# Optimization experiments

Measured on AMD Instinct MI355X. Metric: run time of the kernel, lower is better.

Reference implementation:

```python
import jax, jax.numpy as jnp
import numpy as np

B, S, C, H = 2, 2048, 1024, 16
D = C // H  # head_size = 64


def setup_inputs() -> dict:
    key = jax.random.key(0)
    ks = jax.random.split(key, 8)
    scale = 1.0 / np.sqrt(C)
    return {
        "src": jax.random.normal(ks[0], (B, S, C), dtype=jnp.float32),
        "Wq": jax.random.normal(ks[1], (C, C), dtype=jnp.float32) * scale,
        "bq": jnp.zeros((C,), dtype=jnp.float32),
        "Wk": jax.random.normal(ks[2], (C, C), dtype=jnp.float32) * scale,
        "bk": jnp.zeros((C,), dtype=jnp.float32),
        "Wv": jax.random.normal(ks[3], (C, C), dtype=jnp.float32) * scale,
        "bv": jnp.zeros((C,), dtype=jnp.float32),
        "rel_k_table": jax.random.normal(ks[4], (2 * S - 1, D), dtype=jnp.float32),
    }


def reference(src, Wq, bq, Wk, bk, Wv, bv, rel_k_table):
    # Linear projections (torch Linear: x @ W.T + b)
    q = src @ Wq.T + bq  # (B,S,C)
    k = src @ Wk.T + bk
    v = src @ Wv.T + bv
    # Faithful to torch .view: raw reshape (B,S,C) -> (B,H,S,D), NOT a transpose split
    q = q.reshape(B, H, S, D)
    k = k.reshape(B, H, S, D)
    v = v.reshape(B, H, S, D)
    # content score: q @ k^T
    content = jnp.einsum("bhsd,bhtd->bhst", q, k)  # (B,H,S,S)
    # relative-position embeddings: (S,S,D)
    pos = jnp.arange(S)
    shifted = pos[None, :] - pos[:, None] + (S - 1)  # (S,S) in [0, 2S-2]
    rel_k = rel_k_table[shifted]  # (S,S,D)
    # q.view(S, B*H, D) @ rel_k.permute(0,2,1): batched over first (query-pos) axis
    q_r = q.reshape(S, B * H, D)
    pos_score = jnp.einsum("sbd,std->sbt", q_r, rel_k)  # (S,BH,S)
    pos_score = jnp.transpose(pos_score, (1, 0, 2)).reshape(B, H, S, S)
    scores = (content + pos_score) / jnp.sqrt(jnp.float32(D))
    attn = jax.nn.softmax(scores, axis=-1)
    out = jnp.einsum("bhst,bhtd->bhsd", attn, v)  # (B,H,S,D)
    out = jnp.transpose(out, (0, 2, 1, 3)).reshape(B, S, C)
    return out
```

## Files before the change

kernel.cpp:

```cpp
#include <hip/hip_runtime.h>
#include <hip/hip_bf16.h>

#define BATCH 2
#define SEQ   2048
#define CH    1024
#define NH    16
#define HD    64
#define BHN   (BATCH*NH)
#define SD    (SEQ*HD)

typedef short v8s __attribute__((ext_vector_type(8)));
typedef short v4s __attribute__((ext_vector_type(4)));
typedef float v4f __attribute__((ext_vector_type(4)));

#define VMCNT2() asm volatile("s_waitcnt vmcnt(2)" ::: "memory")
#define VMCNT0() asm volatile("s_waitcnt vmcnt(0)" ::: "memory")
#define SBAR()  do { __builtin_amdgcn_sched_barrier(0); \
                     __builtin_amdgcn_s_barrier();      \
                     __builtin_amdgcn_sched_barrier(0); } while (0)

__device__ __forceinline__ short f2bf(float f) {
    unsigned u = __float_as_uint(f);
    u += 0x7fff + ((u >> 16) & 1);
    return (short)(u >> 16);
}

__device__ __forceinline__ unsigned pk2bf(float a, float b) {
    __hip_bfloat162 h = __float22bfloat162_rn(make_float2(a, b));
    unsigned u;
    __builtin_memcpy(&u, &h, 4);
    return u;
}

__device__ __forceinline__ float ex2(float x) {
    float r; asm("v_exp_f32 %0, %1" : "=v"(r) : "v"(x)); return r;
}

__device__ __forceinline__ void gl_lds16(const short* g, short* l) {
    __builtin_amdgcn_global_load_lds(
        (const __attribute__((address_space(1))) void*)g,
        (__attribute__((address_space(3))) void*)l, 16, 0, 0);
}

__global__ __launch_bounds__(256) void cast_all_kernel(
    const float* __restrict__ src, const float* __restrict__ wq,
    const float* __restrict__ wk, const float* __restrict__ wv,
    const float* __restrict__ rel,
    short* __restrict__ xb, short* __restrict__ wqb,
    short* __restrict__ wkb, short* __restrict__ wvb,
    short* __restrict__ relb)
{
    const int z = blockIdx.z;
    const float* s; short* d; int n4;
    switch (z) {
        case 0: s = src; d = xb;   n4 = 1048576; break;
        case 1: s = wq;  d = wqb;  n4 = 262144;  break;
        case 2: s = wk;  d = wkb;  n4 = 262144;  break;
        case 3: s = wv;  d = wvb;  n4 = 262144;  break;
        default: s = rel; d = relb; n4 = 65520;  break;
    }
    for (int i = blockIdx.x * 256 + threadIdx.x; i < n4; i += gridDim.x * 256) {
        float4 v = ((const float4*)s)[i];
        v4s o; o.x = f2bf(v.x); o.y = f2bf(v.y); o.z = f2bf(v.z); o.w = f2bf(v.w);
        ((v4s*)d)[i] = o;
    }
}

__global__ __launch_bounds__(256, 3) void proj_mfma_kernel(
    const short* __restrict__ Xb,
    const short* __restrict__ Wqb, const short* __restrict__ Wkb,
    const short* __restrict__ Wvb,
    const float* __restrict__ bq, const float* __restrict__ bk,
    const float* __restrict__ bv,
    short* __restrict__ qo, short* __restrict__ ko, short* __restrict__ vo)
{
    const int z = blockIdx.z;
    const short* W    = (z == 0) ? Wqb : (z == 1) ? Wkb : Wvb;
    const float* bias = (z == 0) ? bq  : (z == 1) ? bk  : bv;
    short*       out  = (z == 0) ? qo  : (z == 1) ? ko  : vo;
    const float  osc  = (z == 0) ? 0.125f * 1.44269504088896f : 1.0f;

    const int m0 = blockIdx.x * 128;
    const int n0 = blockIdx.y * 128;
    const int tid  = threadIdx.x;
    const int w    = tid >> 6;
    const int lane = tid & 63;
    const int l15  = lane & 15;
    const int quad = lane >> 4;
    const int wm = w & 1, wn = w >> 1;

    __shared__ short Al[128 * 64];
    __shared__ short Bl[128 * 64];

    v4f acc[4][4];
#pragma unroll
    for (int i = 0; i < 4; i++)
#pragma unroll
        for (int j = 0; j < 4; j++) acc[i][j] = (v4f)(0.f);

    const int srow = tid >> 3;
    const int scol = ((tid & 7) ^ (srow & 7)) * 8;

    int aoff[2][4], boff[2][4];
#pragma unroll
    for (int kk = 0; kk < 2; kk++) {
#pragma unroll
        for (int mt = 0; mt < 4; mt++) {
            const int ra = wm * 64 + mt * 16 + l15;
            aoff[kk][mt] = ra * 64 + ((((kk << 2) | quad) ^ (ra & 7)) << 3);
        }
#pragma unroll
        for (int nt = 0; nt < 4; nt++) {
            const int rb = wn * 64 + nt * 16 + l15;
            boff[kk][nt] = rb * 64 + ((((kk << 2) | quad) ^ (rb & 7)) << 3);
        }
    }

    for (int k0 = 0; k0 < 1024; k0 += 64) {
        __syncthreads();
#pragma unroll
        for (int j = 0; j < 4; j++) {
            gl_lds16(Xb + (size_t)(m0 + j * 32 + srow) * 1024 + k0 + scol,
                     &Al[(j * 32 + w * 8) * 64]);
            gl_lds16(W + (size_t)(n0 + j * 32 + srow) * 1024 + k0 + scol,
                     &Bl[(j * 32 + w * 8) * 64]);
        }
        __syncthreads();
#pragma unroll
        for (int kk = 0; kk < 2; kk++) {
            v8s af[4], bf4[4];
#pragma unroll
            for (int mt = 0; mt < 4; mt++)
                af[mt] = *(const v8s*)&Al[aoff[kk][mt]];
#pragma unroll
            for (int nt = 0; nt < 4; nt++)
                bf4[nt] = *(const v8s*)&Bl[boff[kk][nt]];
#pragma unroll
            for (int mt = 0; mt < 4; mt++)
#pragma unroll
                for (int nt = 0; nt < 4; nt++)
                    acc[mt][nt] = __builtin_amdgcn_mfma_f32_16x16x32_bf16(
                        af[mt], bf4[nt], acc[mt][nt], 0, 0, 0);
        }
    }

    float bv4[4];
#pragma unroll
    for (int nt = 0; nt < 4; nt++)
        bv4[nt] = bias[n0 + wn * 64 + nt * 16 + l15];
#pragma unroll
    for (int mt = 0; mt < 4; mt++)
#pragma unroll
        for (int rg = 0; rg < 4; rg++) {
            const int row = m0 + wm * 64 + mt * 16 + quad * 4 + rg;
#pragma unroll
            for (int nt = 0; nt < 4; nt++)
                out[(size_t)row * 1024 + n0 + wn * 64 + nt * 16 + l15] =
                    f2bf((acc[mt][nt][rg] + bv4[nt]) * osc);
        }
}

__global__ __launch_bounds__(256) void vtrans_kernel(
    const short* __restrict__ v, short* __restrict__ vt)
{
    const int bh = blockIdx.y;
    const int t0 = blockIdx.x * 64;
    const int r = threadIdx.x >> 3;
    const int c = (threadIdx.x & 7) * 8;

    __shared__ short T[64][72];
    *(v8s*)&T[r][c] =
        *(const v8s*)(v + (size_t)bh * SD + (size_t)(t0 + r) * HD + c);
    *(v8s*)&T[r + 32][c] =
        *(const v8s*)(v + (size_t)bh * SD + (size_t)(t0 + r + 32) * HD + c);
    __syncthreads();
    v8s o0, o1;
#pragma unroll
    for (int e = 0; e < 8; e++) {
        const int t = 2 * (threadIdx.x & 7) + (e >> 2) + 16 * (e & 3);
        o0[e] = T[t][r];
        o1[e] = T[t][r + 32];
    }
    *(v8s*)(vt + (size_t)bh * SD + (size_t)r * SEQ + t0 + c) = o0;
    *(v8s*)(vt + (size_t)bh * SD + (size_t)(r + 32) * SEQ + t0 + c) = o1;
}

__global__ __launch_bounds__(256, 2) void attn_mfma_kernel(
    const short* __restrict__ qb, const short* __restrict__ kb,
    const short* __restrict__ vtb, const short* __restrict__ relb,
    float* __restrict__ out)
{
    const int tid  = threadIdx.x;
    const int w    = tid >> 6;
    const int lane = tid & 63;
    const int l15  = lane & 15;
    const int quad = lane >> 4;
    const int bh = blockIdx.x, b = bh >> 4, h = bh & 15;
    const int s0 = blockIdx.y * 128;
    const int i0 = w * 32;

    __shared__ short Kl[2][64][64];
    __shared__ short Vl[2][64][64];
    __shared__ short Rl[256][64];
    __shared__ short Pb[4][2][16][64];

    v8s qc_f[2][2], qr_f[2][2];
#pragma unroll
    for (int mt = 0; mt < 2; mt++)
#pragma unroll
    for (int kh = 0; kh < 2; kh++) {
        const int row = s0 + i0 + mt * 16 + l15;
        qc_f[mt][kh] = *(const v8s*)(qb + (size_t)bh * SD +
                                     (size_t)row * HD + kh * 32 + quad * 8);
        qr_f[mt][kh] = *(const v8s*)(qb + (size_t)row * (BHN * HD) +
                                     bh * HD + kh * 32 + quad * 8);
    }

    int  slv4[4];
    bool slo[4];
    unsigned pwoff[4];
#pragma unroll
    for (int rg = 0; rg < 4; rg++) {
        const int ii = quad * 4 + rg;
        const int e  = l15 + 15 - ii;
        slv4[rg] = (quad * 16 + (e & 15)) << 2;
        slo[rg]  = (l15 >= 15 - ii);
        pwoff[rg] = (unsigned)(w * 4096 + ii * 128 +
                    ((((l15 >> 1) ^ (ii & 7)) << 4) + ((l15 & 1) << 3)));
    }

    const int swz = (quad ^ (l15 & 7)) << 4;
    int kaddr[2][4];
#pragma unroll
    for (int kh = 0; kh < 2; kh++) {
        const int x = kh << 6;
#pragma unroll
        for (int nt = 0; nt < 4; nt++)
            kaddr[kh][nt] = (((nt * 16 + l15) << 7) + swz) ^ x;
    }
    const int paddr0 = (l15 << 7) + swz;

    const int Bq = 1920 - s0;
    int raddr[6];
#pragma unroll
    for (int st = 0; st < 6; st++) {
        const int lg = 2032 - s0 - i0 - 16 + st * 16 + l15;
        raddr[st] = ((lg & 255) << 7) + ((quad ^ (lg & 7)) << 4);
    }

    const int strow = tid >> 3;
    const int stc   = ((tid & 7) ^ (strow & 7)) * 8;
    const short* ksrc = kb  + (size_t)bh * SD + (size_t)strow * HD  + stc;
    const short* vsrc = vtb + (size_t)bh * SD + (size_t)strow * SEQ + stc;

#pragma unroll
    for (int g = 0; g < 3; g++) {
        const int r0 = Bq + g * 64 + strow;
        const int ra = r0 < 4094 ? r0 : 4094;
        const int rb2 = (r0 + 32) < 4094 ? (r0 + 32) : 4094;
        const unsigned sl = (unsigned)((Bq + g * 64 + w * 8) & 255) << 7;
        gl_lds16(relb + (size_t)ra * HD + stc, (short*)((char*)Rl + sl));
        gl_lds16(relb + (size_t)rb2 * HD + stc, (short*)((char*)Rl + sl + 4096));
    }
    gl_lds16(ksrc,              &Kl[0][w * 8][0]);
    gl_lds16(ksrc + 32 * HD,    &Kl[0][32 + w * 8][0]);
    gl_lds16(vsrc,              &Vl[0][w * 8][0]);
    gl_lds16(vsrc + 32 * SEQ,   &Vl[0][32 + w * 8][0]);

    const short* kp = ksrc + 4096;
    const short* vp = vsrc + 64;
    const char*  relbp = (const char*)relb + stc * 2;
    unsigned roff = (unsigned)(Bq + 192 + strow) * 128;
    const unsigned ROMAX = 4094u * 128;
    unsigned rlds = (unsigned)((Bq + 192 + w * 8) & 255) << 7;

    v4f o_acc[2][4];
#pragma unroll
    for (int mt = 0; mt < 2; mt++)
#pragma unroll
        for (int nt = 0; nt < 4; nt++) o_acc[mt][nt] = (v4f)(0.f);
    float lpart[2][4] = {{0.f,0.f,0.f,0.f},{0.f,0.f,0.f,0.f}};

    const v4f vz = (v4f)(0.f);

    v4f cacc[2][4], racc[2][5];
    unsigned g1v[2][4], g2v[2][4];

    auto STAGE_K = [&](int dst) {
        short* kd = &Kl[0][w * 8][0] + (dst << 12);
        gl_lds16(kp,            kd);
        gl_lds16(kp + 32 * HD,  kd + 32 * 64);
        unsigned rc0 = roff < ROMAX ? roff : ROMAX;
        unsigned rc1 = (roff + 4096) < ROMAX ? (roff + 4096) : ROMAX;
        gl_lds16((const short*)(relbp + rc0), (short*)((char*)Rl + rlds));
        gl_lds16((const short*)(relbp + rc1), (short*)((char*)Rl + rlds + 4096));
        kp += 4096; roff += 8192; rlds = (rlds + 8192) & 32767;
    };

    auto STAGE_V = [&](int dst) {
        short* vd = &Vl[0][w * 8][0] + (dst << 12);
        gl_lds16(vp,            vd);
        gl_lds16(vp + 32 * SEQ, vd + 32 * 64);
        vp += 64;
    };

    auto QK = [&](int cur) {
        const char* kbase = (const char*)Kl + cur * 8192;
        const char* rbase = (const char*)Rl;
        {
            v8s kf[4], rfj[6];
#pragma unroll
            for (int nt = 0; nt < 4; nt++)
                kf[nt] = *(const v8s*)(kbase + kaddr[0][nt]);
#pragma unroll
            for (int st = 0; st < 6; st++)
                rfj[st] = *(const v8s*)(rbase + raddr[st]);
            __builtin_amdgcn_s_setprio(1);
#pragma unroll
            for (int mt = 0; mt < 2; mt++)
#pragma unroll
                for (int nt = 0; nt < 4; nt++)
                    cacc[mt][nt] = __builtin_amdgcn_mfma_f32_16x16x32_bf16(
                        qc_f[mt][0], kf[nt], vz, 0, 0, 0);
#pragma unroll
            for (int jt = 0; jt < 5; jt++)
                racc[0][jt] = __builtin_amdgcn_mfma_f32_16x16x32_bf16(
                    qr_f[0][0], rfj[jt + 1], vz, 0, 0, 0);
#pragma unroll
            for (int jt = 0; jt < 5; jt++)
                racc[1][jt] = __builtin_amdgcn_mfma_f32_16x16x32_bf16(
                    qr_f[1][0], rfj[jt], vz, 0, 0, 0);
            __builtin_amdgcn_s_setprio(0);
        }
        {
            v8s kf[4], rfj[6];
#pragma unroll
            for (int nt = 0; nt < 4; nt++)
                kf[nt] = *(const v8s*)(kbase + kaddr[1][nt]);
#pragma unroll
            for (int st = 0; st < 6; st++)
                rfj[st] = *(const v8s*)(rbase + (raddr[st] ^ 64));
            __builtin_amdgcn_s_setprio(1);
#pragma unroll
            for (int mt = 0; mt < 2; mt++)
#pragma unroll
                for (int nt = 0; nt < 4; nt++)
                    cacc[mt][nt] = __builtin_amdgcn_mfma_f32_16x16x32_bf16(
                        qc_f[mt][1], kf[nt], cacc[mt][nt], 0, 0, 0);
#pragma unroll
            for (int jt = 0; jt < 5; jt++)
                racc[0][jt] = __builtin_amdgcn_mfma_f32_16x16x32_bf16(
                    qr_f[0][1], rfj[jt + 1], racc[0][jt], 0, 0, 0);
#pragma unroll
            for (int jt = 0; jt < 5; jt++)
                racc[1][jt] = __builtin_amdgcn_mfma_f32_16x16x32_bf16(
                    qr_f[1][1], rfj[jt], racc[1][jt], 0, 0, 0);
            __builtin_amdgcn_s_setprio(0);
        }
#pragma unroll
        for (int st = 0; st < 6; st++) raddr[st] = (raddr[st] + 8192) & 32767;
    };

    auto PHASE1 = [&]() {
#pragma unroll
        for (int mt = 0; mt < 2; mt++)
#pragma unroll
        for (int rg = 0; rg < 4; rg++) {
            unsigned p01 = pk2bf(racc[mt][0][rg], racc[mt][1][rg]);
            unsigned p12 = pk2bf(racc[mt][1][rg], racc[mt][2][rg]);
            unsigned p23 = pk2bf(racc[mt][2][rg], racc[mt][3][rg]);
            unsigned p34 = pk2bf(racc[mt][3][rg], racc[mt][4][rg]);
            unsigned q1 = slo[rg] ? p01 : p12;
            unsigned q2 = slo[rg] ? p23 : p34;
            g1v[mt][rg] = (unsigned)__builtin_amdgcn_ds_bpermute(slv4[rg], (int)q1);
            g2v[mt][rg] = (unsigned)__builtin_amdgcn_ds_bpermute(slv4[rg], (int)q2);
        }
    };

    auto PHASE2 = [&]() {
#pragma unroll
        for (int mt = 0; mt < 2; mt++)
#pragma unroll
        for (int rg = 0; rg < 4; rg++) {
            const unsigned a1 = g1v[mt][rg], a2 = g2v[mt][rg];
            const unsigned pb0 = a1 << 16;
            const unsigned pb1 = a1 & 0xffff0000u;
            const unsigned pb2 = a2 << 16;
            const unsigned pb3 = a2 & 0xffff0000u;
            float p0 = ex2(cacc[mt][0][rg] + __uint_as_float(pb0));
            float p1 = ex2(cacc[mt][1][rg] + __uint_as_float(pb1));
            float p2 = ex2(cacc[mt][2][rg] + __uint_as_float(pb2));
            float p3 = ex2(cacc[mt][3][rg] + __uint_as_float(pb3));
            lpart[mt][rg] += (p0 + p1) + (p2 + p3);
            *(uint2*)((char*)Pb + pwoff[rg] + mt * 2048) =
                make_uint2(pk2bf(p0, p1), pk2bf(p2, p3));
        }
    };

    auto PV = [&](int vbuf) {
        const char* vbase = (const char*)Vl + vbuf * 8192;
        const char* pbW = (const char*)Pb + w * 4096;
#pragma unroll
        for (int kh = 0; kh < 2; kh++) {
            v8s vf[4];
#pragma unroll
            for (int nt = 0; nt < 4; nt++)
                vf[nt] = *(const v8s*)(vbase + kaddr[kh][nt]);
            v8s pa0 = *(const v8s*)(pbW + (paddr0 ^ (kh << 6)));
            v8s pa1 = *(const v8s*)(pbW + 2048 + (paddr0 ^ (kh << 6)));
            __builtin_amdgcn_s_setprio(1);
#pragma unroll
            for (int nt = 0; nt < 4; nt++)
                o_acc[0][nt] = __builtin_amdgcn_mfma_f32_16x16x32_bf16(
                    pa0, vf[nt], o_acc[0][nt], 0, 0, 0);
#pragma unroll
            for (int nt = 0; nt < 4; nt++)
                o_acc[1][nt] = __builtin_amdgcn_mfma_f32_16x16x32_bf16(
                    pa1, vf[nt], o_acc[1][nt], 0, 0, 0);
            __builtin_amdgcn_s_setprio(0);
        }
    };

    VMCNT0();
    SBAR();
    STAGE_K(1);
    QK(0); PHASE1();
    SBAR();
    STAGE_V(1);
    PHASE2();

    int cur = 0;
    for (int t0 = 64; t0 < SEQ; t0 += 64) {
        cur ^= 1;
        VMCNT2();
        SBAR();
        STAGE_K(cur ^ 1);
        QK(cur);
        PHASE1();
        PV(cur ^ 1);
        SBAR();
        STAGE_V(cur ^ 1);
        PHASE2();
    }
    VMCNT0();
    SBAR();
    PV(cur);

#pragma unroll
    for (int mt = 0; mt < 2; mt++)
#pragma unroll
    for (int rg = 0; rg < 4; rg++) {
        float rs = lpart[mt][rg];
#pragma unroll
        for (int off = 1; off < 16; off <<= 1)
            rs += __shfl_xor(rs, off);
        const float inv = 1.f / rs;
        const int row = s0 + i0 + mt * 16 + quad * 4 + rg;
        const size_t base = ((size_t)b * SEQ + row) * CH + h * HD;
#pragma unroll
        for (int nt = 0; nt < 4; nt++)
            out[base + nt * 16 + l15] = o_acc[mt][nt][rg] * inv;
    }
}

extern "C" void kernel_launch(void* const* d_in, const int* in_sizes, int n_in,
                              void* d_out, int out_size, void* d_ws, size_t ws_size,
                              hipStream_t stream)
{
    const float* src  = (const float*)d_in[0];
    const float* Wq   = (const float*)d_in[1];
    const float* bq   = (const float*)d_in[2];
    const float* Wk   = (const float*)d_in[3];
    const float* bk   = (const float*)d_in[4];
    const float* Wv   = (const float*)d_in[5];
    const float* bv   = (const float*)d_in[6];
    const float* relk = (const float*)d_in[7];
    float* out = (float*)d_out;

    const size_t nQKV = (size_t)BATCH * SEQ * CH;
    const size_t nW   = (size_t)CH * CH;
    short* qb   = (short*)d_ws;
    short* kb   = qb + nQKV;
    short* vb   = kb + nQKV;
    short* vtb  = vb + nQKV;
    short* xb   = vtb + nQKV;
    short* wqb  = xb + nQKV;
    short* wkb  = wqb + nW;
    short* wvb  = wkb + nW;
    short* relb = wvb + nW;

    cast_all_kernel<<<dim3(512, 1, 5), 256, 0, stream>>>(
        src, Wq, Wk, Wv, relk, xb, wqb, wkb, wvb, relb);

    dim3 gProj(4096 / 128, 1024 / 128, 3);
    proj_mfma_kernel<<<gProj, 256, 0, stream>>>(
        xb, wqb, wkb, wvb, bq, bk, bv, qb, kb, vb);

    dim3 gVt(SEQ / 64, BHN);
    vtrans_kernel<<<gVt, 256, 0, stream>>>(vb, vtb);

    dim3 gAttn(BHN, SEQ / 128);
    attn_mfma_kernel<<<gAttn, 256, 0, stream>>>(qb, kb, vtb, relb, out);
}
```

Measured before the change: 203.4 us.

## Load relative-position fragments directly into registers instead of staging through LDS

Drops the 32KB LDS ring that staged rel_k_table rows and its global-to-LDS copies. Each lane now loads its own relative-position MFMA fragments straight from global memory into registers. The loads for the next tile are issued after QK, fenced with sched barriers, so they overlap PHASE1, PV and PHASE2. This removes LDS traffic and capacity for R, at the cost of about 48 extra VGPRs held across the loop and more, less coalesced global/L2 requests per lane.

```diff
diff --git a/kernel.cpp b/kernel.cpp
--- a/kernel.cpp
+++ b/kernel.cpp
@@ -15,6 +15,7 @@
 
 #define VMCNT2() asm volatile("s_waitcnt vmcnt(2)" ::: "memory")
 #define VMCNT0() asm volatile("s_waitcnt vmcnt(0)" ::: "memory")
+#define SCHED0() __builtin_amdgcn_sched_barrier(0)
 #define SBAR()  do { __builtin_amdgcn_sched_barrier(0); \
                      __builtin_amdgcn_s_barrier();      \
                      __builtin_amdgcn_sched_barrier(0); } while (0)
@@ -201,7 +202,6 @@
 
     __shared__ short Kl[2][64][64];
     __shared__ short Vl[2][64][64];
-    __shared__ short Rl[256][64];
     __shared__ short Pb[4][2][16][64];
 
     v8s qc_f[2][2], qr_f[2][2];
@@ -240,39 +240,39 @@
     }
     const int paddr0 = (l15 << 7) + swz;
 
-    const int Bq = 1920 - s0;
-    int raddr[6];
+    unsigned roffs[6];
 #pragma unroll
     for (int st = 0; st < 6; st++) {
         const int lg = 2032 - s0 - i0 - 16 + st * 16 + l15;
-        raddr[st] = ((lg & 255) << 7) + ((quad ^ (lg & 7)) << 4);
-    }
+        roffs[st] = (unsigned)lg * HD;
+    }
+    const unsigned RMAX = 4094u * HD;
+
+    v8s rfp[6][2];
+    auto LOAD_R = [&]() {
+#pragma unroll
+        for (int st = 0; st < 6; st++) {
+            const unsigned c = roffs[st] < RMAX ? roffs[st] : RMAX;
+            const short* p = relb + c + quad * 8;
+            rfp[st][0] = *(const v8s*)(p);
+            rfp[st][1] = *(const v8s*)(p + 32);
+            roffs[st] += 64 * HD;
+        }
+    };
 
     const int strow = tid >> 3;
     const int stc   = ((tid & 7) ^ (strow & 7)) * 8;
     const short* ksrc = kb  + (size_t)bh * SD + (size_t)strow * HD  + stc;
     const short* vsrc = vtb + (size_t)bh * SD + (size_t)strow * SEQ + stc;
 
-#pragma unroll
-    for (int g = 0; g < 3; g++) {
-        const int r0 = Bq + g * 64 + strow;
-        const int ra = r0 < 4094 ? r0 : 4094;
-        const int rb2 = (r0 + 32) < 4094 ? (r0 + 32) : 4094;
-        const unsigned sl = (unsigned)((Bq + g * 64 + w * 8) & 255) << 7;
-        gl_lds16(relb + (size_t)ra * HD + stc, (short*)((char*)Rl + sl));
-        gl_lds16(relb + (size_t)rb2 * HD + stc, (short*)((char*)Rl + sl + 4096));
-    }
     gl_lds16(ksrc,              &Kl[0][w * 8][0]);
     gl_lds16(ksrc + 32 * HD,    &Kl[0][32 + w * 8][0]);
     gl_lds16(vsrc,              &Vl[0][w * 8][0]);
     gl_lds16(vsrc + 32 * SEQ,   &Vl[0][32 + w * 8][0]);
+    LOAD_R();
 
     const short* kp = ksrc + 4096;
     const short* vp = vsrc + 64;
-    const char*  relbp = (const char*)relb + stc * 2;
-    unsigned roff = (unsigned)(Bq + 192 + strow) * 128;
-    const unsigned ROMAX = 4094u * 128;
-    unsigned rlds = (unsigned)((Bq + 192 + w * 8) & 255) << 7;
 
     v4f o_acc[2][4];
 #pragma unroll
@@ -290,11 +290,7 @@
         short* kd = &Kl[0][w * 8][0] + (dst << 12);
         gl_lds16(kp,            kd);
         gl_lds16(kp + 32 * HD,  kd + 32 * 64);
-        unsigned rc0 = roff < ROMAX ? roff : ROMAX;
-        unsigned rc1 = (roff + 4096) < ROMAX ? (roff + 4096) : ROMAX;
-        gl_lds16((const short*)(relbp + rc0), (short*)((char*)Rl + rlds));
-        gl_lds16((const short*)(relbp + rc1), (short*)((char*)Rl + rlds + 4096));
-        kp += 4096; roff += 8192; rlds = (rlds + 8192) & 32767;
+        kp += 4096;
     };
 
     auto STAGE_V = [&](int dst) {
@@ -306,15 +302,11 @@
 
     auto QK = [&](int cur) {
         const char* kbase = (const char*)Kl + cur * 8192;
-        const char* rbase = (const char*)Rl;
         {
-            v8s kf[4], rfj[6];
+            v8s kf[4];
 #pragma unroll
             for (int nt = 0; nt < 4; nt++)
                 kf[nt] = *(const v8s*)(kbase + kaddr[0][nt]);
-#pragma unroll
-            for (int st = 0; st < 6; st++)
-                rfj[st] = *(const v8s*)(rbase + raddr[st]);
             __builtin_amdgcn_s_setprio(1);
 #pragma unroll
             for (int mt = 0; mt < 2; mt++)
@@ -325,21 +317,18 @@
 #pragma unroll
             for (int jt = 0; jt < 5; jt++)
                 racc[0][jt] = __builtin_amdgcn_mfma_f32_16x16x32_bf16(
-                    qr_f[0][0], rfj[jt + 1], vz, 0, 0, 0);
+                    qr_f[0][0], rfp[jt + 1][0], vz, 0, 0, 0);
 #pragma unroll
             for (int jt = 0; jt < 5; jt++)
                 racc[1][jt] = __builtin_amdgcn_mfma_f32_16x16x32_bf16(
-                    qr_f[1][0], rfj[jt], vz, 0, 0, 0);
+                    qr_f[1][0], rfp[jt][0], vz, 0, 0, 0);
             __builtin_amdgcn_s_setprio(0);
         }
         {
-            v8s kf[4], rfj[6];
+            v8s kf[4];
 #pragma unroll
             for (int nt = 0; nt < 4; nt++)
                 kf[nt] = *(const v8s*)(kbase + kaddr[1][nt]);
-#pragma unroll
-            for (int st = 0; st < 6; st++)
-                rfj[st] = *(const v8s*)(rbase + (raddr[st] ^ 64));
             __builtin_amdgcn_s_setprio(1);
 #pragma unroll
             for (int mt = 0; mt < 2; mt++)
@@ -350,15 +339,13 @@
 #pragma unroll
             for (int jt = 0; jt < 5; jt++)
                 racc[0][jt] = __builtin_amdgcn_mfma_f32_16x16x32_bf16(
-                    qr_f[0][1], rfj[jt + 1], racc[0][jt], 0, 0, 0);
+                    qr_f[0][1], rfp[jt + 1][1], racc[0][jt], 0, 0, 0);
 #pragma unroll
             for (int jt = 0; jt < 5; jt++)
                 racc[1][jt] = __builtin_amdgcn_mfma_f32_16x16x32_bf16(
-                    qr_f[1][1], rfj[jt], racc[1][jt], 0, 0, 0);
+                    qr_f[1][1], rfp[jt][1], racc[1][jt], 0, 0, 0);
             __builtin_amdgcn_s_setprio(0);
         }
-#pragma unroll
-        for (int st = 0; st < 6; st++) raddr[st] = (raddr[st] + 8192) & 32767;
     };
 
     auto PHASE1 = [&]() {
@@ -424,7 +411,9 @@
     VMCNT0();
     SBAR();
     STAGE_K(1);
-    QK(0); PHASE1();
+    QK(0);
+    SCHED0(); LOAD_R(); SCHED0();
+    PHASE1();
     SBAR();
     STAGE_V(1);
     PHASE2();
@@ -436,6 +425,7 @@
         SBAR();
         STAGE_K(cur ^ 1);
         QK(cur);
+        SCHED0(); LOAD_R(); SCHED0();
         PHASE1();
         PV(cur ^ 1);
         SBAR();
```

Measured after the change: 240.3 us. 18.1% more time.
